# Kernel optimization log

Measured on AMD Instinct MI355X. Metric: run time of the kernel, lower is better.

Reference implementation:

```python
import jax, jax.numpy as jnp
import numpy as np

N_EMBD = 512
N_HEAD = 8
HEAD_DIM = N_EMBD // N_HEAD  # 64
SCALE = HEAD_DIM ** -0.5


def setup_inputs() -> dict:
    key = jax.random.key(0)
    k1, k2, k3 = jax.random.split(key, 3)
    x = jax.random.normal(k1, (2, 2048, N_EMBD), dtype=jnp.float32)
    # torch Linear(n_embd, 3*n_embd, bias=False) -> store as (in, out): y = x @ W
    w_attn = jax.random.normal(k2, (N_EMBD, 3 * N_EMBD), dtype=jnp.float32) * 0.02
    w_proj = jax.random.normal(k3, (N_EMBD, N_EMBD), dtype=jnp.float32) * 0.02
    return {"x": x, "w_attn": w_attn, "w_proj": w_proj}


def reference(x, w_attn, w_proj):
    B, T, C = x.shape
    qkv = x @ w_attn                                   # (B, T, 3C)
    q, k, v = jnp.split(qkv, 3, axis=-1)
    q = q.reshape(B, T, N_HEAD, HEAD_DIM).transpose(0, 2, 1, 3)  # (B,H,T,D)
    k = k.reshape(B, T, N_HEAD, HEAD_DIM).transpose(0, 2, 1, 3)
    v = v.reshape(B, T, N_HEAD, HEAD_DIM).transpose(0, 2, 1, 3)
    # FAITHFUL to source: `weights.fill_(float('-inf'))` overwrites q@k^T*scale
    # in-place, then triu(diagonal=1) keeps -inf strictly above the diagonal and
    # zeros elsewhere. q/k scores are DISCARDED by the original code.
    # Resulting softmax weights are identical across batch/head, so compute a
    # single (T, T) matrix instead of materializing (B, H, T, T).
    mask = jnp.triu(jnp.full((T, T), -jnp.inf, dtype=x.dtype), 1)  # -inf above diag, 0 else
    w = jax.nn.softmax(mask, axis=-1)                  # uniform over positions <= i
    attn = jnp.einsum('ts,bhsd->bhtd', w, v)           # causal running mean of v
    attn = attn.transpose(0, 2, 1, 3).reshape(B, T, C)
    y = attn @ w_proj
    return y
```

## Files before the change

kernel.cpp:

```cpp
#include <hip/hip_runtime.h>

typedef __bf16 bf16x8 __attribute__((ext_vector_type(8)));
typedef float  f32x4  __attribute__((ext_vector_type(4)));

__device__ __forceinline__ unsigned short f2bf(float f) {
    unsigned int u = __float_as_uint(f);
    u += 0x7FFF + ((u >> 16) & 1);
    return (unsigned short)(u >> 16);
}

#define GLD_LDS16(gptr, lptr) \
    __builtin_amdgcn_global_load_lds((const __attribute__((address_space(1))) void*)(gptr), \
                                     (__attribute__((address_space(3))) void*)(lptr), 16, 0, 0)

template<int EPI>
__device__ __forceinline__ void gemm_tile(const unsigned short* __restrict__ A,
                                          const unsigned short* __restrict__ Bt,
                                          void* __restrict__ Cout,
                                          unsigned short* lds,
                                          int bm, int bn)
{
    const int tid  = threadIdx.x;
    const int lane = tid & 63;
    const int w    = tid >> 6;
    const int wm   = w >> 1, wn = w & 1;

    const int srow   = w * 16 + (lane >> 3);
    const int schunk = (lane & 7) ^ (lane >> 3);
    const unsigned short* gA0 = A  + (size_t)(bm + srow    ) * 512 + schunk * 8;
    const unsigned short* gA1 = A  + (size_t)(bm + srow + 8) * 512 + schunk * 8;
    const unsigned short* gB0 = Bt + (size_t)(bn + srow    ) * 512 + schunk * 8;
    const unsigned short* gB1 = Bt + (size_t)(bn + srow + 8) * 512 + schunk * 8;

    const int arow = lane & 15;
    const int kg   = lane >> 4;
    int offA[2][2], offB[2][2];
    #pragma unroll
    for (int f = 0; f < 2; ++f)
        #pragma unroll
        for (int kk = 0; kk < 2; ++kk) {
            offA[f][kk] = (wm * 32 + f * 16 + arow) * 128 + (((kk * 4 + kg) ^ (arow & 7)) << 4);
            offB[f][kk] = (wn * 32 + f * 16 + arow) * 128 + (((kk * 4 + kg) ^ (arow & 7)) << 4);
        }

    f32x4 acc[2][2] = {};

    auto stage = [&](int buf, int kt) {
        const int k0 = kt * 64;
        unsigned short* la = lds + buf * 8192;
        unsigned short* lb = la + 4096;
        GLD_LDS16(gA0 + k0, la + (w * 16 + 0) * 64);
        GLD_LDS16(gA1 + k0, la + (w * 16 + 8) * 64);
        GLD_LDS16(gB0 + k0, lb + (w * 16 + 0) * 64);
        GLD_LDS16(gB1 + k0, lb + (w * 16 + 8) * 64);
    };

    stage(0, 0);
    asm volatile("s_waitcnt vmcnt(0)" ::: "memory");
    __syncthreads();

    #pragma unroll
    for (int kt = 0; kt < 8; ++kt) {
        const int buf = kt & 1;
        if (kt < 7) stage(buf ^ 1, kt + 1);
        const char* la = (const char*)(lds + buf * 8192);
        const char* lb = la + 8192;
        #pragma unroll
        for (int kk = 0; kk < 2; ++kk) {
            bf16x8 a0 = *(const bf16x8*)(la + offA[0][kk]);
            bf16x8 a1 = *(const bf16x8*)(la + offA[1][kk]);
            bf16x8 b0 = *(const bf16x8*)(lb + offB[0][kk]);
            bf16x8 b1 = *(const bf16x8*)(lb + offB[1][kk]);
            acc[0][0] = __builtin_amdgcn_mfma_f32_16x16x32_bf16(a0, b0, acc[0][0], 0, 0, 0);
            acc[0][1] = __builtin_amdgcn_mfma_f32_16x16x32_bf16(a0, b1, acc[0][1], 0, 0, 0);
            acc[1][0] = __builtin_amdgcn_mfma_f32_16x16x32_bf16(a1, b0, acc[1][0], 0, 0, 0);
            acc[1][1] = __builtin_amdgcn_mfma_f32_16x16x32_bf16(a1, b1, acc[1][1], 0, 0, 0);
        }
        asm volatile("s_waitcnt vmcnt(0)" ::: "memory");
        __syncthreads();
    }

    #pragma unroll
    for (int fm = 0; fm < 2; ++fm)
        #pragma unroll
        for (int fn = 0; fn < 2; ++fn) {
            const int row0 = bm + wm * 32 + fm * 16 + kg * 4;
            const int col  = bn + wn * 32 + fn * 16 + arow;
            if (EPI == 0) {
                float* C = (float*)Cout;
                #pragma unroll
                for (int r = 0; r < 4; ++r)
                    C[(size_t)(row0 + r) * 512 + col] = acc[fm][fn][r];
            } else {
                unsigned short* C = (unsigned short*)Cout;
                ushort4 pk;
                pk.x = f2bf(acc[fm][fn][0]);
                pk.y = f2bf(acc[fm][fn][1]);
                pk.z = f2bf(acc[fm][fn][2]);
                pk.w = f2bf(acc[fm][fn][3]);
                *(ushort4*)(&C[(size_t)col * 512 + row0]) = pk;
            }
        }
}

__global__ __launch_bounds__(256) void k1_prep_partial(
    const float* __restrict__ x, const float* __restrict__ w_attn,
    const float* __restrict__ w_proj,
    unsigned short* __restrict__ wv, unsigned short* __restrict__ wpT,
    float* __restrict__ part)
{
    __shared__ float ls[64][65];
    const int bid = blockIdx.x, tid = threadIdx.x;

    if (bid < 64) {
        const int m0 = (bid >> 3) * 64;
        const int j0 = (bid & 7) * 64;
        const int rr = tid >> 4;
        const int c4 = (tid & 15) * 4;
        #pragma unroll
        for (int i = 0; i < 4; ++i) {
            float4 v = *(const float4*)(w_proj + (size_t)(m0 + rr + 16 * i) * 512 + j0 + c4);
            ls[rr + 16 * i][c4 + 0] = v.x;
            ls[rr + 16 * i][c4 + 1] = v.y;
            ls[rr + 16 * i][c4 + 2] = v.z;
            ls[rr + 16 * i][c4 + 3] = v.w;
        }
        __syncthreads();
        const int c    = tid >> 2;
        const int mgrp = (tid & 3) * 16;
        #pragma unroll
        for (int u = 0; u < 4; ++u) {
            const int m = mgrp + u * 4;
            ushort4 o;
            o.x = f2bf(ls[m + 0][c]);
            o.y = f2bf(ls[m + 1][c]);
            o.z = f2bf(ls[m + 2][c]);
            o.w = f2bf(ls[m + 3][c]);
            *(ushort4*)(wpT + (size_t)(j0 + c) * 512 + m0 + m) = o;
        }
    } else if (bid < 128) {
        const int bb = bid - 64;
        #pragma unroll
        for (int i = 0; i < 4; ++i) {
            const int flat = bb * 1024 + i * 256 + tid;
            const int ir = flat >> 7;
            const int m4 = (flat & 127) * 4;
            float4 v = *(const float4*)(w_attn + (size_t)ir * 1536 + 1024 + m4);
            ushort4 o;
            o.x = f2bf(v.x); o.y = f2bf(v.y); o.z = f2bf(v.z); o.w = f2bf(v.w);
            *(ushort4*)(wv + (size_t)ir * 512 + m4) = o;
        }
    } else {
        const int bx = bid - 128;
        const int b  = bx >> 7;
        const int ch = (bx >> 1) & 63;
        const int j  = (bx & 1) * 256 + tid;
        const float* p = x + ((size_t)b * 2048 + ch * 32) * 512 + j;
        float s = 0.f;
        #pragma unroll 8
        for (int t = 0; t < 32; ++t) s += p[(size_t)t * 512];
        part[((size_t)b * 64 + ch) * 512 + j] = s;
    }
}

__global__ __launch_bounds__(256) void k2_smallgemm_finalize(
    const float* __restrict__ x,
    const unsigned short* __restrict__ wv, const unsigned short* __restrict__ wpT,
    const float* __restrict__ part,
    unsigned short* __restrict__ wcT, unsigned short* __restrict__ s16)
{
    __shared__ unsigned short lds[2 * 2 * 4096];
    const int bid = blockIdx.x, tid = threadIdx.x;

    if (bid < 64) {
        gemm_tile<1>(wv, wpT, wcT, lds, (bid >> 3) * 64, (bid & 7) * 64);
    } else {
        const int bx = bid - 64;
        const int b  = bx >> 7;
        const int ch = (bx >> 1) & 63;
        const int j  = (bx & 1) * 256 + tid;
        float run = 0.f;
        #pragma unroll 8
        for (int cc = 0; cc < 63; ++cc) {
            float v = part[((size_t)b * 64 + cc) * 512 + j];
            run += (cc < ch) ? v : 0.f;
        }
        const float*    p = x   + ((size_t)b * 2048 + ch * 32) * 512 + j;
        unsigned short* q = s16 + ((size_t)b * 2048 + ch * 32) * 512 + j;
        #pragma unroll 8
        for (int t = 0; t < 32; ++t) {
            run += p[(size_t)t * 512];
            q[(size_t)t * 512] = f2bf(run * (1.0f / (float)(ch * 32 + t + 1)));
        }
    }
}

__global__ __launch_bounds__(256) void k3_biggemm(
    const unsigned short* __restrict__ s16,
    const unsigned short* __restrict__ wcT,
    float* __restrict__ y)
{
    __shared__ unsigned short lds[2 * 2 * 4096];
    const int bid  = blockIdx.x;
    const int xcd  = bid & 7;
    const int idx  = bid >> 3;
    const int vy   = xcd * 8 + (idx >> 3);
    const int vx   = idx & 7;
    gemm_tile<0>(s16, wcT, y, lds, vy * 64, vx * 64);
}

extern "C" void kernel_launch(void* const* d_in, const int* in_sizes, int n_in,
                              void* d_out, int out_size, void* d_ws, size_t ws_size,
                              hipStream_t stream)
{
    const float* x      = (const float*)d_in[0];
    const float* w_attn = (const float*)d_in[1];
    const float* w_proj = (const float*)d_in[2];
    float* y = (float*)d_out;

    unsigned short* wv  = (unsigned short*)d_ws;
    unsigned short* wpT = wv  + 512 * 512;
    unsigned short* wcT = wpT + 512 * 512;
    unsigned short* s16 = wcT + 512 * 512;
    float* part = (float*)(s16 + (size_t)4096 * 512);

    k1_prep_partial<<<384, 256, 0, stream>>>(x, w_attn, w_proj, wv, wpT, part);
    k2_smallgemm_finalize<<<320, 256, 0, stream>>>(x, wv, wpT, part, wcT, s16);
    k3_biggemm<<<512, 256, 0, stream>>>(s16, wcT, y);
}
```

Measured before the change: 25.97 us.

## Double K-tile depth and keep two stages in flight in GEMM tile

The shared GEMM tile now stages 128-wide K slices instead of 64 and cuts the K loop from 8 to 4 iterations. It issues two stages up front and waits with a partial vmcnt, so the next tile's global-to-LDS loads overlap the current tile's MFMAs. The swizzle is widened to 16 chunks and LDS doubles to 64 KB per block. This halves the number of barriers and deepens prefetch, at the cost of more LDS, which may reduce occupancy.

```diff
diff --git a/kernel.cpp b/kernel.cpp
--- a/kernel.cpp
+++ b/kernel.cpp
@@ -24,49 +24,48 @@
     const int lane = tid & 63;
     const int w    = tid >> 6;
     const int wm   = w >> 1, wn = w & 1;
-
-    const int srow   = w * 16 + (lane >> 3);
-    const int schunk = (lane & 7) ^ (lane >> 3);
-    const unsigned short* gA0 = A  + (size_t)(bm + srow    ) * 512 + schunk * 8;
-    const unsigned short* gA1 = A  + (size_t)(bm + srow + 8) * 512 + schunk * 8;
-    const unsigned short* gB0 = Bt + (size_t)(bn + srow    ) * 512 + schunk * 8;
-    const unsigned short* gB1 = Bt + (size_t)(bn + srow + 8) * 512 + schunk * 8;
-
     const int arow = lane & 15;
     const int kg   = lane >> 4;
-    int offA[2][2], offB[2][2];
+
+    const int srow   = tid >> 4;
+    const int schunk = (tid & 15) ^ srow;
+    const unsigned short* gA = A  + (size_t)(bm + srow) * 512 + schunk * 8;
+    const unsigned short* gB = Bt + (size_t)(bn + srow) * 512 + schunk * 8;
+
+    auto stage = [&](int buf, int kt) {
+        unsigned short* la = lds + buf * 16384;
+        unsigned short* lb = la + 8192;
+        const int k0 = kt * 128;
+        #pragma unroll
+        for (int i = 0; i < 4; ++i) {
+            GLD_LDS16(gA + (size_t)(i * 16) * 512 + k0, la + i * 2048 + w * 512);
+            GLD_LDS16(gB + (size_t)(i * 16) * 512 + k0, lb + i * 2048 + w * 512);
+        }
+    };
+
+    int offA[2][4], offB[2][4];
     #pragma unroll
     for (int f = 0; f < 2; ++f)
         #pragma unroll
-        for (int kk = 0; kk < 2; ++kk) {
-            offA[f][kk] = (wm * 32 + f * 16 + arow) * 128 + (((kk * 4 + kg) ^ (arow & 7)) << 4);
-            offB[f][kk] = (wn * 32 + f * 16 + arow) * 128 + (((kk * 4 + kg) ^ (arow & 7)) << 4);
-        }
+        for (int kk = 0; kk < 4; ++kk) {
+            offA[f][kk] = (wm * 32 + f * 16 + arow) * 256 + (((kk * 4 + kg) ^ arow) << 4);
+            offB[f][kk] = (wn * 32 + f * 16 + arow) * 256 + (((kk * 4 + kg) ^ arow) << 4);
+        }
+
+    stage(0, 0);
+    stage(1, 1);
 
     f32x4 acc[2][2] = {};
-
-    auto stage = [&](int buf, int kt) {
-        const int k0 = kt * 64;
-        unsigned short* la = lds + buf * 8192;
-        unsigned short* lb = la + 4096;
-        GLD_LDS16(gA0 + k0, la + (w * 16 + 0) * 64);
-        GLD_LDS16(gA1 + k0, la + (w * 16 + 8) * 64);
-        GLD_LDS16(gB0 + k0, lb + (w * 16 + 0) * 64);
-        GLD_LDS16(gB1 + k0, lb + (w * 16 + 8) * 64);
-    };
-
-    stage(0, 0);
-    asm volatile("s_waitcnt vmcnt(0)" ::: "memory");
-    __syncthreads();
-
     #pragma unroll
-    for (int kt = 0; kt < 8; ++kt) {
+    for (int kt = 0; kt < 4; ++kt) {
         const int buf = kt & 1;
-        if (kt < 7) stage(buf ^ 1, kt + 1);
-        const char* la = (const char*)(lds + buf * 8192);
-        const char* lb = la + 8192;
-        #pragma unroll
-        for (int kk = 0; kk < 2; ++kk) {
+        if (kt < 3) asm volatile("s_waitcnt vmcnt(8)" ::: "memory");
+        else        asm volatile("s_waitcnt vmcnt(0)" ::: "memory");
+        __builtin_amdgcn_s_barrier();
+        const char* la = (const char*)(lds + buf * 16384);
+        const char* lb = la + 16384;
+        #pragma unroll
+        for (int kk = 0; kk < 4; ++kk) {
             bf16x8 a0 = *(const bf16x8*)(la + offA[0][kk]);
             bf16x8 a1 = *(const bf16x8*)(la + offA[1][kk]);
             bf16x8 b0 = *(const bf16x8*)(lb + offB[0][kk]);
@@ -76,8 +75,8 @@
             acc[1][0] = __builtin_amdgcn_mfma_f32_16x16x32_bf16(a1, b0, acc[1][0], 0, 0, 0);
             acc[1][1] = __builtin_amdgcn_mfma_f32_16x16x32_bf16(a1, b1, acc[1][1], 0, 0, 0);
         }
-        asm volatile("s_waitcnt vmcnt(0)" ::: "memory");
-        __syncthreads();
+        __builtin_amdgcn_s_barrier();
+        if (kt < 2) stage(buf, kt + 2);
     }
 
     #pragma unroll
@@ -169,7 +168,7 @@
     const float* __restrict__ part,
     unsigned short* __restrict__ wcT, unsigned short* __restrict__ s16)
 {
-    __shared__ unsigned short lds[2 * 2 * 4096];
+    __shared__ __align__(16) unsigned short lds[2 * 16384];
     const int bid = blockIdx.x, tid = threadIdx.x;
 
     if (bid < 64) {
@@ -200,7 +199,7 @@
     const unsigned short* __restrict__ wcT,
     float* __restrict__ y)
 {
-    __shared__ unsigned short lds[2 * 2 * 4096];
+    __shared__ __align__(16) unsigned short lds[2 * 16384];
     const int bid  = blockIdx.x;
     const int xcd  = bid & 7;
     const int idx  = bid >> 3;
```

New measurement: 24.73 us. -4.8%, faster.

## Merge finalize and big GEMM into one kernel with flag-based dataflow sync

Applied to the files above, without the earlier changes.

Folds the third kernel into the second: the big-GEMM blocks now spin on global atomic flags until the weight-combine GEMM and their 64-row slice of the scan are done, instead of waiting for a kernel boundary. Flags are zeroed by an extra block in the first kernel. The scan blocks also process two columns per thread with float2 loads and packed bf16 stores, halving the block count. This removes one launch and lets GEMM tiles start as soon as their inputs are ready. In exchange it relies on producer blocks being scheduled before spinning consumers (704 blocks with launch_bounds occupancy 4), which risks deadlock or spin overhead.

```diff
diff --git a/kernel.cpp b/kernel.cpp
--- a/kernel.cpp
+++ b/kernel.cpp
@@ -8,10 +8,17 @@
     u += 0x7FFF + ((u >> 16) & 1);
     return (unsigned short)(u >> 16);
 }
+__device__ __forceinline__ unsigned int pk2bf(float a, float b) {
+    return (unsigned int)f2bf(a) | ((unsigned int)f2bf(b) << 16);
+}
 
 #define GLD_LDS16(gptr, lptr) \
     __builtin_amdgcn_global_load_lds((const __attribute__((address_space(1))) void*)(gptr), \
                                      (__attribute__((address_space(3))) void*)(lptr), 16, 0, 0)
+
+#define FWC 0
+#define FMT(mt) (16 + 16 * (mt))
+#define NFLAGS (16 + 16 * 64)
 
 template<int EPI>
 __device__ __forceinline__ void gemm_tile(const unsigned short* __restrict__ A,
@@ -107,7 +114,7 @@
     const float* __restrict__ x, const float* __restrict__ w_attn,
     const float* __restrict__ w_proj,
     unsigned short* __restrict__ wv, unsigned short* __restrict__ wpT,
-    float* __restrict__ part)
+    float* __restrict__ part, int* __restrict__ flags)
 {
     __shared__ float ls[64][65];
     const int bid = blockIdx.x, tid = threadIdx.x;
@@ -150,63 +157,77 @@
             o.x = f2bf(v.x); o.y = f2bf(v.y); o.z = f2bf(v.z); o.w = f2bf(v.w);
             *(ushort4*)(wv + (size_t)ir * 512 + m4) = o;
         }
+    } else if (bid < 256) {
+        const int g  = bid - 128;
+        const int k0 = tid * 2;
+        const float* p = x + (size_t)g * 32 * 512 + k0;
+        float rx = 0.f, ry = 0.f;
+        #pragma unroll 8
+        for (int t = 0; t < 32; ++t) {
+            float2 v = *(const float2*)(p + (size_t)t * 512);
+            rx += v.x; ry += v.y;
+        }
+        *(float2*)(part + (size_t)g * 512 + k0) = make_float2(rx, ry);
     } else {
-        const int bx = bid - 128;
-        const int b  = bx >> 7;
-        const int ch = (bx >> 1) & 63;
-        const int j  = (bx & 1) * 256 + tid;
-        const float* p = x + ((size_t)b * 2048 + ch * 32) * 512 + j;
-        float s = 0.f;
-        #pragma unroll 8
-        for (int t = 0; t < 32; ++t) s += p[(size_t)t * 512];
-        part[((size_t)b * 64 + ch) * 512 + j] = s;
+        for (int i = tid; i < NFLAGS; i += 256) flags[i] = 0;
     }
 }
 
-__global__ __launch_bounds__(256) void k2_smallgemm_finalize(
+__global__ __launch_bounds__(256, 4) void k2_merged(
     const float* __restrict__ x,
     const unsigned short* __restrict__ wv, const unsigned short* __restrict__ wpT,
     const float* __restrict__ part,
-    unsigned short* __restrict__ wcT, unsigned short* __restrict__ s16)
-{
-    __shared__ unsigned short lds[2 * 2 * 4096];
+    unsigned short* __restrict__ wcT, unsigned short* __restrict__ s16,
+    float* __restrict__ y, int* __restrict__ flags)
+{
+    __shared__ __align__(16) unsigned short lds[2 * 2 * 4096];
     const int bid = blockIdx.x, tid = threadIdx.x;
 
     if (bid < 64) {
         gemm_tile<1>(wv, wpT, wcT, lds, (bid >> 3) * 64, (bid & 7) * 64);
-    } else {
-        const int bx = bid - 64;
-        const int b  = bx >> 7;
-        const int ch = (bx >> 1) & 63;
-        const int j  = (bx & 1) * 256 + tid;
-        float run = 0.f;
+        __threadfence();
+        __syncthreads();
+        if (tid == 0)
+            __hip_atomic_fetch_add(&flags[FWC], 1, __ATOMIC_RELEASE, __HIP_MEMORY_SCOPE_AGENT);
+    } else if (bid < 192) {
+        const int g  = bid - 64;
+        const int b  = g >> 6, ch = g & 63;
+        const int k0 = tid * 2;
+        float rx = 0.f, ry = 0.f;
         #pragma unroll 8
         for (int cc = 0; cc < 63; ++cc) {
-            float v = part[((size_t)b * 64 + cc) * 512 + j];
-            run += (cc < ch) ? v : 0.f;
-        }
-        const float*    p = x   + ((size_t)b * 2048 + ch * 32) * 512 + j;
-        unsigned short* q = s16 + ((size_t)b * 2048 + ch * 32) * 512 + j;
+            float2 v = *(const float2*)(part + ((size_t)b * 64 + cc) * 512 + k0);
+            rx += (cc < ch) ? v.x : 0.f;
+            ry += (cc < ch) ? v.y : 0.f;
+        }
+        const float*    p = x   + (size_t)g * 32 * 512 + k0;
+        unsigned short* q = s16 + (size_t)g * 32 * 512 + k0;
         #pragma unroll 8
         for (int t = 0; t < 32; ++t) {
-            run += p[(size_t)t * 512];
-            q[(size_t)t * 512] = f2bf(run * (1.0f / (float)(ch * 32 + t + 1)));
-        }
+            float2 v = *(const float2*)(p + (size_t)t * 512);
+            rx += v.x; ry += v.y;
+            const float inv = 1.0f / (float)(ch * 32 + t + 1);
+            *(unsigned int*)(q + (size_t)t * 512) = pk2bf(rx * inv, ry * inv);
+        }
+        __threadfence();
+        __syncthreads();
+        if (tid == 0)
+            __hip_atomic_fetch_add(&flags[FMT(g >> 1)], 1, __ATOMIC_RELEASE, __HIP_MEMORY_SCOPE_AGENT);
+    } else {
+        const int ii  = bid - 192;
+        const int xcd = ii & 7, idx = ii >> 3;
+        const int vy  = xcd * 8 + (idx >> 3);
+        const int vx  = idx & 7;
+        if (tid == 0) {
+            while (__hip_atomic_load(&flags[FWC], __ATOMIC_RELAXED, __HIP_MEMORY_SCOPE_AGENT) < 64)
+                __builtin_amdgcn_s_sleep(2);
+            while (__hip_atomic_load(&flags[FMT(vy)], __ATOMIC_RELAXED, __HIP_MEMORY_SCOPE_AGENT) < 2)
+                __builtin_amdgcn_s_sleep(2);
+        }
+        __syncthreads();
+        __threadfence();
+        gemm_tile<0>(s16, wcT, y, lds, vy * 64, vx * 64);
     }
-}
-
-__global__ __launch_bounds__(256) void k3_biggemm(
-    const unsigned short* __restrict__ s16,
-    const unsigned short* __restrict__ wcT,
-    float* __restrict__ y)
-{
-    __shared__ unsigned short lds[2 * 2 * 4096];
-    const int bid  = blockIdx.x;
-    const int xcd  = bid & 7;
-    const int idx  = bid >> 3;
-    const int vy   = xcd * 8 + (idx >> 3);
-    const int vx   = idx & 7;
-    gemm_tile<0>(s16, wcT, y, lds, vy * 64, vx * 64);
 }
 
 extern "C" void kernel_launch(void* const* d_in, const int* in_sizes, int n_in,
@@ -223,8 +244,8 @@
     unsigned short* wcT = wpT + 512 * 512;
     unsigned short* s16 = wcT + 512 * 512;
     float* part = (float*)(s16 + (size_t)4096 * 512);
-
-    k1_prep_partial<<<384, 256, 0, stream>>>(x, w_attn, w_proj, wv, wpT, part);
-    k2_smallgemm_finalize<<<320, 256, 0, stream>>>(x, wv, wpT, part, wcT, s16);
-    k3_biggemm<<<512, 256, 0, stream>>>(s16, wcT, y);
-}
+    int*   flags = (int*)(part + 128 * 512);
+
+    k1_prep_partial<<<257, 256, 0, stream>>>(x, w_attn, w_proj, wv, wpT, part, flags);
+    k2_merged<<<704, 256, 0, stream>>>(x, wv, wpT, part, wcT, s16, y, flags);
+}
```

After: 86.26 us. 232% more time.
